# Kernel tuning notes

Measured on AMD Instinct MI355X. Metric: run time of the kernel, lower is better.

The kernel has to match this reference:

```python
import jax, jax.numpy as jnp
import numpy as np

DIL = 2  # dilation of the 3x3 neighborhood (hardcoded in the torch module)
# 8 non-center neighbor offsets of a dilated 3x3 kernel
_OFFSETS = [(-DIL, -DIL), (-DIL, 0), (-DIL, DIL),
            (0, -DIL),              (0, DIL),
            (DIL, -DIL), (DIL, 0),  (DIL, DIL)]


def setup_inputs() -> dict:
    key = jax.random.key(0)
    k1, k2 = jax.random.split(key)
    shape = (16, 1, 1024, 1024)
    y_true = jax.random.uniform(k1, shape, dtype=jnp.float32)
    y_pred = jax.random.uniform(k2, shape, dtype=jnp.float32)
    return {"y_true": y_true, "y_pred": y_pred}


def reference(y_true, y_pred):
    # --- BCE with torch's log clamp at -100 (reduction='none') ---
    log_p  = jnp.maximum(jnp.log(y_pred),   -100.0)
    log_1p = jnp.maximum(jnp.log1p(-y_pred), -100.0)
    a = -(y_true * log_p + (1.0 - y_true) * log_1p)

    # --- detached copy (y_pred.clone().detach()) ---
    sloss = jax.lax.stop_gradient(y_pred)

    # --- max |center - neighbor| over 8 dilated neighbors, zero-padded borders ---
    H, W = sloss.shape[2], sloss.shape[3]
    padded = jnp.pad(sloss, ((0, 0), (0, 0), (DIL, DIL), (DIL, DIL)))
    unfolded_weights = jnp.zeros_like(sloss)
    for dy, dx in _OFFSETS:
        nb = padded[:, :, DIL + dy:DIL + dy + H, DIL + dx:DIL + dx + W]
        unfolded_weights = jnp.maximum(unfolded_weights, jnp.abs(sloss - nb))

    # thred[thred < 0.5] = 0; loss1 uses thred BEFORE the >=0.5 -> 1 assignment
    thred = jnp.where(sloss >= 0.5, sloss, 0.0)
    loss = unfolded_weights * thred + a
    return loss.mean()
```

## Files before the change

kernel.cpp:

```cpp
#include <hip/hip_runtime.h>

#define HH 1024
#define WW 1024
#define NB 16
#define NROWS (NB * HH)
#define NELEM ((long long)NROWS * WW)

__device__ __forceinline__ void load_row(const float* __restrict__ rowp, int x0,
                                         bool ledge, bool redge,
                                         int offL, int offR, float w[8]) {
    float2 a = *(const float2*)(rowp + offL);
    float4 b = *(const float4*)(rowp + x0);
    float2 c = *(const float2*)(rowp + offR);
    if (ledge) { a.x = 0.f; a.y = 0.f; }
    if (redge) { c.x = 0.f; c.y = 0.f; }
    w[0]=a.x; w[1]=a.y; w[2]=b.x; w[3]=b.y; w[4]=b.z; w[5]=b.w; w[6]=c.x; w[7]=c.y;
}

__device__ __forceinline__ void zero_row(float w[8]) {
#pragma unroll
    for (int i = 0; i < 8; ++i) w[i] = 0.f;
}

__global__ __launch_bounds__(256) void closs_main(const float* __restrict__ yt,
                                                  const float* __restrict__ yp,
                                                  float* __restrict__ partial) {
    const int bid = blockIdx.x;
    const int r   = ((bid & 7) << 11) | (bid >> 3);
    const int y   = r & (HH - 1);
    const int tid = threadIdx.x;
    const int x0  = tid << 2;
    const long long rowbase = (long long)r * WW;

    const bool ledge = (tid == 0);
    const bool redge = (tid == 255);
    const int offL = ledge ? x0 : (x0 - 2);
    const int offR = redge ? x0 : (x0 + 4);

    const float* pce = yp + rowbase;

    float A[8], B[8], C[8];
    load_row(pce, x0, ledge, redge, offL, offR, B);
    if (y >= 2) load_row(pce - 2 * WW, x0, ledge, redge, offL, offR, A);
    else        zero_row(A);
    if (y < HH - 2) load_row(pce + 2 * WW, x0, ledge, redge, offL, offR, C);
    else            zero_row(C);

    const float4 t4 = *(const float4*)(yt + rowbase + x0);
    const float tt[4] = {t4.x, t4.y, t4.z, t4.w};

    float sum = 0.f;
#pragma unroll
    for (int j = 0; j < 4; ++j) {
        const float c = B[j + 2];
        const float mxA = fmaxf(fmaxf(A[j], A[j + 2]), A[j + 4]);
        const float mxB = fmaxf(B[j], B[j + 4]);
        const float mxC = fmaxf(fmaxf(C[j], C[j + 2]), C[j + 4]);
        const float mx  = fmaxf(fmaxf(mxA, mxB), mxC);
        const float mnA = fminf(fminf(A[j], A[j + 2]), A[j + 4]);
        const float mnB = fminf(B[j], B[j + 4]);
        const float mnC = fminf(fminf(C[j], C[j + 2]), C[j + 4]);
        const float mn  = fminf(fminf(mnA, mnB), mnC);
        const float w   = fmaxf(mx - c, c - mn);

        const float lp  = fmaxf(__logf(c), -100.f);
        const float l1p = fmaxf(__logf(1.f - c), -100.f);
        const float th  = (c >= 0.5f) ? c : 0.f;
        sum += w * th - l1p - tt[j] * (lp - l1p);
    }

    for (int o = 32; o > 0; o >>= 1) sum += __shfl_down(sum, o);
    __shared__ float wsum[4];
    if ((tid & 63) == 0) wsum[tid >> 6] = sum;
    __syncthreads();
    if (tid == 0) partial[r] = wsum[0] + wsum[1] + wsum[2] + wsum[3];
}

__global__ __launch_bounds__(1024) void closs_reduce(const float* __restrict__ partial,
                                                     float* __restrict__ out) {
    const float4* p4 = (const float4*)partial;
    float s = 0.f;
#pragma unroll
    for (int i = 0; i < 4; ++i) {
        float4 v = p4[threadIdx.x + (i << 10)];
        s += (v.x + v.y) + (v.z + v.w);
    }
    for (int o = 32; o > 0; o >>= 1) s += __shfl_down(s, o);
    __shared__ float wsum[16];
    if ((threadIdx.x & 63) == 0) wsum[threadIdx.x >> 6] = s;
    __syncthreads();
    if (threadIdx.x == 0) {
        float t = 0.f;
#pragma unroll
        for (int i = 0; i < 16; ++i) t += wsum[i];
        out[0] = t * (1.0f / (float)NELEM);
    }
}

extern "C" void kernel_launch(void* const* d_in, const int* in_sizes, int n_in,
                              void* d_out, int out_size, void* d_ws, size_t ws_size,
                              hipStream_t stream) {
    const float* y_true = (const float*)d_in[0];
    const float* y_pred = (const float*)d_in[1];
    float* out = (float*)d_out;
    float* partial = (float*)d_ws;

    closs_main<<<NROWS, 256, 0, stream>>>(y_true, y_pred, partial);
    closs_reduce<<<1, 1024, 0, stream>>>(partial, out);
}
```

Measured before the change: 152.8 us.

## Tile 8 rows per block with shared-memory halo staging of y_pred

Each block now handles an 8-row tile, staging 12 rows of y_pred (tile plus 2-row halo on each side) into shared memory once and reading the dilated neighborhoods from LDS. Before, each row-block loaded its own three rows from global memory, which tripled y_pred reads through the cache. The reduction kernel shrinks to match the 2048 partials. Costs are 48KB of LDS per block, which limits occupancy, a barrier after staging, and possible LDS bank conflicts on the offset float2 reads.

```diff
diff --git a/kernel.cpp b/kernel.cpp
--- a/kernel.cpp
+++ b/kernel.cpp
@@ -3,88 +3,93 @@
 #define HH 1024
 #define WW 1024
 #define NB 16
-#define NROWS (NB * HH)
-#define NELEM ((long long)NROWS * WW)
+#define TR 8
+#define SR (TR + 4)
+#define NBLK (NB * (HH / TR))
+#define NELEM ((long long)NB * HH * WW)
 
-__device__ __forceinline__ void load_row(const float* __restrict__ rowp, int x0,
-                                         bool ledge, bool redge,
-                                         int offL, int offR, float w[8]) {
-    float2 a = *(const float2*)(rowp + offL);
-    float4 b = *(const float4*)(rowp + x0);
-    float2 c = *(const float2*)(rowp + offR);
-    if (ledge) { a.x = 0.f; a.y = 0.f; }
-    if (redge) { c.x = 0.f; c.y = 0.f; }
-    w[0]=a.x; w[1]=a.y; w[2]=b.x; w[3]=b.y; w[4]=b.z; w[5]=b.w; w[6]=c.x; w[7]=c.y;
-}
-
-__device__ __forceinline__ void zero_row(float w[8]) {
-#pragma unroll
-    for (int i = 0; i < 8; ++i) w[i] = 0.f;
+__device__ __forceinline__ void lds_win(const float* __restrict__ S, int row,
+                                        int c0, bool ledge, bool redge, float w[8]) {
+    const float* p = S + row * WW;
+    float2 L = *(const float2*)(p + (ledge ? c0 : c0 - 2));
+    float4 M = *(const float4*)(p + c0);
+    float2 R = *(const float2*)(p + (redge ? c0 : c0 + 4));
+    if (ledge) { L.x = 0.f; L.y = 0.f; }
+    if (redge) { R.x = 0.f; R.y = 0.f; }
+    w[0]=L.x; w[1]=L.y; w[2]=M.x; w[3]=M.y; w[4]=M.z; w[5]=M.w; w[6]=R.x; w[7]=R.y;
 }
 
 __global__ __launch_bounds__(256) void closs_main(const float* __restrict__ yt,
                                                   const float* __restrict__ yp,
                                                   float* __restrict__ partial) {
-    const int bid = blockIdx.x;
-    const int r   = ((bid & 7) << 11) | (bid >> 3);
-    const int y   = r & (HH - 1);
-    const int tid = threadIdx.x;
-    const int x0  = tid << 2;
-    const long long rowbase = (long long)r * WW;
+    __shared__ float S[SR * WW];
+
+    const int bid  = blockIdx.x;
+    const int img  = bid >> 7;
+    const int tile = bid & 127;
+    const int y0   = tile * TR;
+    const int tid  = threadIdx.x;
+    const int c0   = tid << 2;
+
+    const float* __restrict__ ybase = yp + (long long)img * (HH * WW);
+    const float* __restrict__ tbase = yt + ((long long)img * HH + y0) * WW;
+
+#pragma unroll
+    for (int i = 0; i < SR; ++i) {
+        const int gy = y0 - 2 + i;
+        float4 v = make_float4(0.f, 0.f, 0.f, 0.f);
+        if (gy >= 0 && gy < HH)
+            v = *(const float4*)(ybase + gy * WW + c0);
+        *(float4*)&S[i * WW + c0] = v;
+    }
+    __syncthreads();
 
     const bool ledge = (tid == 0);
     const bool redge = (tid == 255);
-    const int offL = ledge ? x0 : (x0 - 2);
-    const int offR = redge ? x0 : (x0 + 4);
-
-    const float* pce = yp + rowbase;
-
-    float A[8], B[8], C[8];
-    load_row(pce, x0, ledge, redge, offL, offR, B);
-    if (y >= 2) load_row(pce - 2 * WW, x0, ledge, redge, offL, offR, A);
-    else        zero_row(A);
-    if (y < HH - 2) load_row(pce + 2 * WW, x0, ledge, redge, offL, offR, C);
-    else            zero_row(C);
-
-    const float4 t4 = *(const float4*)(yt + rowbase + x0);
-    const float tt[4] = {t4.x, t4.y, t4.z, t4.w};
 
     float sum = 0.f;
 #pragma unroll
-    for (int j = 0; j < 4; ++j) {
-        const float c = B[j + 2];
-        const float mxA = fmaxf(fmaxf(A[j], A[j + 2]), A[j + 4]);
-        const float mxB = fmaxf(B[j], B[j + 4]);
-        const float mxC = fmaxf(fmaxf(C[j], C[j + 2]), C[j + 4]);
-        const float mx  = fmaxf(fmaxf(mxA, mxB), mxC);
-        const float mnA = fminf(fminf(A[j], A[j + 2]), A[j + 4]);
-        const float mnB = fminf(B[j], B[j + 4]);
-        const float mnC = fminf(fminf(C[j], C[j + 2]), C[j + 4]);
-        const float mn  = fminf(fminf(mnA, mnB), mnC);
-        const float w   = fmaxf(mx - c, c - mn);
+    for (int k = 0; k < TR; ++k) {
+        float A[8], B[8], C[8];
+        lds_win(S, k,     c0, ledge, redge, A);
+        lds_win(S, k + 2, c0, ledge, redge, B);
+        lds_win(S, k + 4, c0, ledge, redge, C);
 
-        const float lp  = fmaxf(__logf(c), -100.f);
-        const float l1p = fmaxf(__logf(1.f - c), -100.f);
-        const float th  = (c >= 0.5f) ? c : 0.f;
-        sum += w * th - l1p - tt[j] * (lp - l1p);
+        const float4 t4 = *(const float4*)(tbase + k * WW + c0);
+        const float tt[4] = {t4.x, t4.y, t4.z, t4.w};
+
+#pragma unroll
+        for (int j = 0; j < 4; ++j) {
+            const float c = B[j + 2];
+            const float mxA = fmaxf(fmaxf(A[j], A[j + 2]), A[j + 4]);
+            const float mxB = fmaxf(B[j], B[j + 4]);
+            const float mxC = fmaxf(fmaxf(C[j], C[j + 2]), C[j + 4]);
+            const float mx  = fmaxf(fmaxf(mxA, mxB), mxC);
+            const float mnA = fminf(fminf(A[j], A[j + 2]), A[j + 4]);
+            const float mnB = fminf(B[j], B[j + 4]);
+            const float mnC = fminf(fminf(C[j], C[j + 2]), C[j + 4]);
+            const float mn  = fminf(fminf(mnA, mnB), mnC);
+            const float w   = fmaxf(mx - c, c - mn);
+
+            const float lp  = fmaxf(__logf(c), -100.f);
+            const float l1p = fmaxf(__logf(1.f - c), -100.f);
+            const float th  = (c >= 0.5f) ? c : 0.f;
+            sum += w * th - l1p - tt[j] * (lp - l1p);
+        }
     }
 
     for (int o = 32; o > 0; o >>= 1) sum += __shfl_down(sum, o);
     __shared__ float wsum[4];
     if ((tid & 63) == 0) wsum[tid >> 6] = sum;
     __syncthreads();
-    if (tid == 0) partial[r] = wsum[0] + wsum[1] + wsum[2] + wsum[3];
+    if (tid == 0) partial[bid] = wsum[0] + wsum[1] + wsum[2] + wsum[3];
 }
 
 __global__ __launch_bounds__(1024) void closs_reduce(const float* __restrict__ partial,
                                                      float* __restrict__ out) {
-    const float4* p4 = (const float4*)partial;
-    float s = 0.f;
-#pragma unroll
-    for (int i = 0; i < 4; ++i) {
-        float4 v = p4[threadIdx.x + (i << 10)];
-        s += (v.x + v.y) + (v.z + v.w);
-    }
+    const float2* p2 = (const float2*)partial;
+    float2 v = p2[threadIdx.x];
+    float s = v.x + v.y;
     for (int o = 32; o > 0; o >>= 1) s += __shfl_down(s, o);
     __shared__ float wsum[16];
     if ((threadIdx.x & 63) == 0) wsum[threadIdx.x >> 6] = s;
@@ -105,6 +110,6 @@
     float* out = (float*)d_out;
     float* partial = (float*)d_ws;
 
-    closs_main<<<NROWS, 256, 0, stream>>>(y_true, y_pred, partial);
+    closs_main<<<NBLK, 256, 0, stream>>>(y_true, y_pred, partial);
     closs_reduce<<<1, 1024, 0, stream>>>(partial, out);
 }
```

Result: faster. 146.5 us (-4.1%).
